# Kernel optimization log

Measured on AMD Instinct MI355X. Metric: run time of the kernel, lower is better.

## Reference

```python
import jax, jax.numpy as jnp
import numpy as np

B, T, C, L = 1024, 256, 128, 64
NEG = -1e30  # finite stand-in for -inf (safe gradients)
EPS = 1e-7   # keras.backend.epsilon()


def setup_inputs() -> dict:
    key = jax.random.key(0)
    k1, k2 = jax.random.split(key)
    # y_pred is a softmax output (probabilities), as keras ctc_batch_cost expects
    logits = jax.random.normal(k1, (B, T, C), dtype=jnp.float32)
    y_pred = jax.nn.softmax(logits, axis=-1)
    # labels in [0, C-2]; class C-1 is the CTC blank (keras convention)
    y_true = jax.random.randint(k2, (B, L), 0, C - 1, dtype=jnp.int64)
    return {"y_true": y_true, "y_pred": y_pred}


def ctc_loss(y_true, y_pred):
    """Negative log-likelihood CTC loss per sample, shape [B, 1].
    Matches keras.backend.ctc_batch_cost with full input/label lengths,
    blank index = num_classes - 1, log(y_pred + eps)."""
    Bb, Tt, Cc = y_pred.shape
    Ll = y_true.shape[1]
    blank = Cc - 1
    S = 2 * Ll + 1  # extended label: blank, l1, blank, l2, ..., blank

    logp = jnp.log(y_pred + EPS)  # [B, T, C]

    ext = jnp.full((Bb, S), blank, dtype=y_true.dtype).at[:, 1::2].set(y_true)  # [B, S]
    # per-(t, s) log-prob of the extended symbol: lp[b, t, s] = logp[b, t, ext[b, s]]
    lp = jnp.take_along_axis(logp, ext[:, None, :], axis=2)  # [B, T, S]

    # skip transition s-2 -> s allowed iff ext[s] != blank and ext[s] != ext[s-2]
    ext_m2 = jnp.concatenate(
        [jnp.full((Bb, 2), blank, dtype=ext.dtype), ext[:, :-2]], axis=1)
    can_skip = (ext != blank) & (ext != ext_m2)  # [B, S]

    def shift1(a):
        return jnp.concatenate(
            [jnp.full((Bb, 1), NEG, dtype=a.dtype), a[:, :-1]], axis=1)

    # alpha init at t=0: only s=0 (blank) and s=1 (first label) reachable
    alpha0 = (jnp.full((Bb, S), NEG, dtype=lp.dtype)
              .at[:, 0].set(lp[:, 0, 0])
              .at[:, 1].set(lp[:, 0, 1]))

    def step(alpha, lp_t):
        a1 = shift1(alpha)
        a2 = jnp.where(can_skip, shift1(shift1(alpha)), NEG)
        new = jax.nn.logsumexp(jnp.stack([alpha, a1, a2], axis=0), axis=0) + lp_t
        return new, None

    lp_tbs = jnp.swapaxes(lp, 0, 1)  # [T, B, S]
    alpha, _ = jax.lax.scan(step, alpha0, lp_tbs[1:])

    log_lik = jnp.logaddexp(alpha[:, S - 1], alpha[:, S - 2])  # end on last blank or last label
    return -log_lik[:, None]  # [B, 1], matching ctc_batch_cost output shape


def reference(y_true, y_pred):
    return ctc_loss(y_true, y_pred)
```

## Files before the change

### kernel.cpp

```cpp
#include <hip/hip_runtime.h>
#include <math.h>


#define Bn 1024
#define Tn 256
#define Cn 128
#define Ln 64
#define BLANK 127
#define U 8
#define NC (Tn / U)
#define EPS128 (1e-7f * 128.0f)
#define LN2 0.69314718055994530942f

template <int CTRL>
__device__ __forceinline__ float dpp_movf(float x) {
    return __int_as_float(__builtin_amdgcn_update_dpp(
        0, __float_as_int(x), CTRL, 0xF, 0xF, true));
}
__device__ __forceinline__ int dpp_shr1_i(int x) {
    return __builtin_amdgcn_update_dpp(0, x, 0x138, 0xF, 0xF, true);
}

__global__ __launch_bounds__(64)
void ctc_lds_kernel(const int* __restrict__ y_true,
                    const float* __restrict__ y_pred,
                    float* __restrict__ out) {
    const int b = blockIdx.x;
    const int i = threadIdx.x;

    __shared__ __align__(16) float prob[2][U * Cn];

    const int li = y_true[b * Ln + i];
    const int ll = dpp_shr1_i(li);
    const float skf = (li != ll) ? 1.0f : 0.0f;

    const float4* gsrc = (const float4*)(y_pred + (size_t)b * (Tn * Cn));
    float4 ra[4], rb[4];

    auto gload = [&](int c, float4* r) {
        const float4* p = gsrc + c * (U * Cn / 4) + i;
#pragma unroll
        for (int k = 0; k < 4; ++k) r[k] = p[k * 64];
    };
    auto lwrite = [&](int buf, const float4* r) {
        float4* d = ((float4*)prob[buf]) + i;
#pragma unroll
        for (int k = 0; k < 4; ++k) d[k * 64] = r[k];
    };

    float E = 0.f, O = 0.f, X = 0.f;
    int Esum = 0;

    auto steps = [&](const float* pr, bool first) {
#pragma unroll
        for (int j = 0; j < U; ++j) {
            const float* row = pr + j * Cn;
            const float ql = fmaf(row[li],    128.0f, EPS128);
            const float qb = fmaf(row[BLANK], 128.0f, EPS128);
            if (first && j == 0) {
                E = (i == 0) ? qb : 0.f;
                O = (i == 0) ? ql : 0.f;
                X = 0.f;
                continue;
            }
            const float Ol = dpp_movf<0x138>(O);
            const float t1 = O + E;
            const float nO = fmaf(skf, Ol, t1) * ql;
            const float nE = (E + Ol) * qb;
            const float nX = (X + O) * qb;
            E = nE; O = nO; X = nX;
        }
    };
    auto renorm = [&]() {
        float m = fmaxf(E, O);
        if (i == 63) m = fmaxf(m, X);
        m = fmaxf(m, dpp_movf<0x111>(m));
        m = fmaxf(m, dpp_movf<0x112>(m));
        m = fmaxf(m, dpp_movf<0x114>(m));
        m = fmaxf(m, dpp_movf<0x118>(m));
        m = fmaxf(m, dpp_movf<0x142>(m));
        m = fmaxf(m, dpp_movf<0x143>(m));
        const unsigned ub =
            (unsigned)__builtin_amdgcn_readlane(__float_as_int(m), 63);
        const int eb = (int)(ub >> 23);
        const float sc = __int_as_float((unsigned)(254 - eb) << 23);
        Esum += eb - 127;
        E *= sc; O *= sc; X *= sc;
    };

    gload(0, ra);
    gload(1, rb);
    lwrite(0, ra);
    gload(2, ra);

    for (int c = 0; c < NC; c += 2) {
        lwrite(1, rb);
        if (c + 3 < NC) gload(c + 3, rb);
        steps(prob[0], c == 0);
        renorm();
        lwrite(0, ra);
        if (c + 4 < NC) gload(c + 4, ra);
        steps(prob[1], false);
        if (c + 2 < NC) renorm();
    }

    if (i == 63) {
        const float s = O + X;
#if __has_builtin(__builtin_amdgcn_logf)
        const float l2 = __builtin_amdgcn_logf(s);
#else
        const float l2 = log2f(s);
#endif
        out[b] = -(l2 + (float)(Esum - 7 * Tn)) * LN2;
    }
}

extern "C" void kernel_launch(void* const* d_in, const int* in_sizes, int n_in,
                              void* d_out, int out_size, void* d_ws, size_t ws_size,
                              hipStream_t stream) {
    const int*   y_true = (const int*)d_in[0];
    const float* y_pred = (const float*)d_in[1];
    float*       out    = (float*)d_out;
    hipLaunchKernelGGL(ctc_lds_kernel, dim3(Bn), dim3(64), 0, stream,
                       y_true, y_pred, out);
}
```

Measured before the change: 207.3 us.

## Replace register-staged double buffer with async global-to-LDS ring prefetch

The kernel now streams y_pred chunks straight into an 8-slot LDS ring with global_load_lds DMA, keeping 7 chunks in flight, where before it staged them through registers into a 2-slot buffer. Each chunk's label and blank probabilities are read from LDS into registers one chunk ahead of the recurrence, so LDS reads overlap the serial alpha steps. The aim is deeper memory-level parallelism and less register traffic on a latency-bound serial scan. In exchange it uses 32KB of LDS per block, which can lower occupancy, and it relies on hand-placed vmcnt waits and scheduling barriers. There is no explicit LDS barrier, since each block is a single wavefront.

```diff
diff --git a/kernel.cpp b/kernel.cpp
--- a/kernel.cpp
+++ b/kernel.cpp
@@ -9,8 +9,13 @@
 #define BLANK 127
 #define U 8
 #define NC (Tn / U)
+#define RING 8
+#define DEPTH 7
 #define EPS128 (1e-7f * 128.0f)
 #define LN2 0.69314718055994530942f
+
+#define WAIT_VM(n) __builtin_amdgcn_s_waitcnt((((n) & 0xF) | (((n) >> 4) << 14)) | 0x0F70)
+#define SCHED_FENCE() __builtin_amdgcn_sched_barrier(0)
 
 template <int CTRL>
 __device__ __forceinline__ float dpp_movf(float x) {
@@ -20,54 +25,61 @@
 __device__ __forceinline__ int dpp_shr1_i(int x) {
     return __builtin_amdgcn_update_dpp(0, x, 0x138, 0xF, 0xF, true);
 }
+__device__ __forceinline__ void dma16(const float* g, float* l) {
+    __builtin_amdgcn_global_load_lds(
+        (const __attribute__((address_space(1))) void*)g,
+        (__attribute__((address_space(3))) void*)l, 16, 0, 0);
+}
 
 __global__ __launch_bounds__(64)
-void ctc_lds_kernel(const int* __restrict__ y_true,
-                    const float* __restrict__ y_pred,
-                    float* __restrict__ out) {
+void ctc_ring_kernel(const int* __restrict__ y_true,
+                     const float* __restrict__ y_pred,
+                     float* __restrict__ out) {
+    __shared__ __align__(16) float ring[RING][U * Cn];
     const int b = blockIdx.x;
     const int i = threadIdx.x;
-
-    __shared__ __align__(16) float prob[2][U * Cn];
 
     const int li = y_true[b * Ln + i];
     const int ll = dpp_shr1_i(li);
     const float skf = (li != ll) ? 1.0f : 0.0f;
 
-    const float4* gsrc = (const float4*)(y_pred + (size_t)b * (Tn * Cn));
-    float4 ra[4], rb[4];
+    const float* gb = y_pred + (size_t)b * (Tn * Cn);
 
-    auto gload = [&](int c, float4* r) {
-        const float4* p = gsrc + c * (U * Cn / 4) + i;
+    auto issue_chunk = [&](int c) {
+        const float* g = gb + c * (U * Cn);
+        float* l = ring[c & (RING - 1)];
 #pragma unroll
-        for (int k = 0; k < 4; ++k) r[k] = p[k * 64];
+        for (int k = 0; k < 4; ++k)
+            dma16(g + k * 256 + i * 4, l + k * 256);
     };
-    auto lwrite = [&](int buf, const float4* r) {
-        float4* d = ((float4*)prob[buf]) + i;
+
+    float qlA[U], qbA[U], qlB[U], qbB[U];
+    auto qread = [&](int c, float* ql, float* qb) {
+        const float* s = ring[c & (RING - 1)];
 #pragma unroll
-        for (int k = 0; k < 4; ++k) d[k * 64] = r[k];
+        for (int j = 0; j < U; ++j) {
+            ql[j] = fmaf(s[j * Cn + li],    128.0f, EPS128);
+            qb[j] = fmaf(s[j * Cn + BLANK], 128.0f, EPS128);
+        }
     };
 
     float E = 0.f, O = 0.f, X = 0.f;
     int Esum = 0;
 
-    auto steps = [&](const float* pr, bool first) {
+    auto steps = [&](const float* ql, const float* qb, bool first) {
 #pragma unroll
         for (int j = 0; j < U; ++j) {
-            const float* row = pr + j * Cn;
-            const float ql = fmaf(row[li],    128.0f, EPS128);
-            const float qb = fmaf(row[BLANK], 128.0f, EPS128);
             if (first && j == 0) {
-                E = (i == 0) ? qb : 0.f;
-                O = (i == 0) ? ql : 0.f;
+                E = (i == 0) ? qb[0] : 0.f;
+                O = (i == 0) ? ql[0] : 0.f;
                 X = 0.f;
                 continue;
             }
             const float Ol = dpp_movf<0x138>(O);
             const float t1 = O + E;
-            const float nO = fmaf(skf, Ol, t1) * ql;
-            const float nE = (E + Ol) * qb;
-            const float nX = (X + O) * qb;
+            const float nO = fmaf(skf, Ol, t1) * ql[j];
+            const float nE = (E + Ol) * qb[j];
+            const float nX = (X + O) * qb[j];
             E = nE; O = nO; X = nX;
         }
     };
@@ -88,21 +100,39 @@
         E *= sc; O *= sc; X *= sc;
     };
 
-    gload(0, ra);
-    gload(1, rb);
-    lwrite(0, ra);
-    gload(2, ra);
+#pragma unroll
+    for (int c = 0; c < DEPTH; ++c) issue_chunk(c);
+    WAIT_VM(24);
+    SCHED_FENCE();
+    qread(0, qlA, qbA);
 
-    for (int c = 0; c < NC; c += 2) {
-        lwrite(1, rb);
-        if (c + 3 < NC) gload(c + 3, rb);
-        steps(prob[0], c == 0);
+    for (int cc = 0; cc < 24; cc += 2) {
+        WAIT_VM(20); SCHED_FENCE();
+        qread(cc + 1, qlB, qbB);
+        issue_chunk(cc + 7);
+        steps(qlA, qbA, cc == 0);
         renorm();
-        lwrite(0, ra);
-        if (c + 4 < NC) gload(c + 4, ra);
-        steps(prob[1], false);
-        if (c + 2 < NC) renorm();
+        WAIT_VM(20); SCHED_FENCE();
+        qread(cc + 2, qlA, qbA);
+        issue_chunk(cc + 8);
+        steps(qlB, qbB, false);
+        renorm();
     }
+    WAIT_VM(20); SCHED_FENCE();
+    qread(25, qlB, qbB);
+    issue_chunk(31);
+    steps(qlA, qbA, false);
+    renorm();
+    WAIT_VM(0); SCHED_FENCE();
+    qread(26, qlA, qbA);
+    steps(qlB, qbB, false);
+    renorm();
+    qread(27, qlB, qbB); steps(qlA, qbA, false); renorm();
+    qread(28, qlA, qbA); steps(qlB, qbB, false); renorm();
+    qread(29, qlB, qbB); steps(qlA, qbA, false); renorm();
+    qread(30, qlA, qbA); steps(qlB, qbB, false); renorm();
+    qread(31, qlB, qbB); steps(qlA, qbA, false); renorm();
+    steps(qlB, qbB, false);
 
     if (i == 63) {
         const float s = O + X;
@@ -121,6 +151,6 @@
     const int*   y_true = (const int*)d_in[0];
     const float* y_pred = (const float*)d_in[1];
     float*       out    = (float*)d_out;
-    hipLaunchKernelGGL(ctc_lds_kernel, dim3(Bn), dim3(64), 0, stream,
+    hipLaunchKernelGGL(ctc_ring_kernel, dim3(Bn), dim3(64), 0, stream,
                        y_true, y_pred, out);
 }
```

New measurement: 191.9 us. 7.5% less time.
